# Kernel tuning notes

Measured on AMD Instinct MI355X. Metric: run time of the kernel, lower is better.

The kernel has to match this reference:

```python
import jax, jax.numpy as jnp
import numpy as np

D = 256; NH = 8; DH = D // NH; NL = 4; NP = 4; DFFN = 1024
SPATIAL = [(128, 128), (64, 64), (32, 32), (16, 16)]
LEN_IN = sum(h * w for h, w in SPATIAL)
N, LQ = 8, 1000


def _ln(x, g, b, eps=1e-5):
    m = jnp.mean(x, -1, keepdims=True)
    v = jnp.mean((x - m) ** 2, -1, keepdims=True)
    return (x - m) * jax.lax.rsqrt(v + eps) * g + b


def _ms_deform_core(value, loc, attn_w):
    # value (N,Len_in,NH,DH); loc (N,Lq,NH,NL,NP,2) in [0,1]; attn_w (N,Lq,NH,NL,NP)
    n, lq = loc.shape[0], loc.shape[1]
    out = jnp.zeros((n, NH, lq, DH), value.dtype)
    start = 0
    for l, (Hl, Wl) in enumerate(SPATIAL):
        v = value[:, start:start + Hl * Wl].transpose(0, 2, 1, 3)  # (N,NH,HW,DH)
        start += Hl * Wl
        # grid_sample-style mapping, align_corners=False, zero padding
        x = loc[:, :, :, l, :, 0] * Wl - 0.5  # (N,Lq,NH,NP)
        y = loc[:, :, :, l, :, 1] * Hl - 0.5
        x0 = jnp.floor(x); y0 = jnp.floor(y)
        lx = x - x0; ly = y - y0
        x0i = x0.astype(jnp.int32); y0i = y0.astype(jnp.int32)
        acc = jnp.zeros((n, NH, lq, NP, DH), value.dtype)
        for dy, dx, w in ((0, 0, (1 - ly) * (1 - lx)), (0, 1, (1 - ly) * lx),
                          (1, 0, ly * (1 - lx)), (1, 1, ly * lx)):
            xi = x0i + dx; yi = y0i + dy
            valid = ((xi >= 0) & (xi < Wl) & (yi >= 0) & (yi < Hl)).astype(value.dtype)
            idx = jnp.clip(yi, 0, Hl - 1) * Wl + jnp.clip(xi, 0, Wl - 1)  # (N,Lq,NH,NP)
            idx = idx.transpose(0, 2, 1, 3).reshape(n, NH, lq * NP)
            g = jnp.take_along_axis(v, idx[..., None], axis=2).reshape(n, NH, lq, NP, DH)
            acc = acc + g * (w * valid).transpose(0, 2, 1, 3)[..., None]
        out = out + jnp.sum(acc * attn_w[:, :, :, l].transpose(0, 2, 1, 3)[..., None], axis=3)
    return out.transpose(0, 2, 1, 3).reshape(n, lq, D)


def setup_inputs() -> dict:
    key = jax.random.key(0)
    ks = jax.random.split(key, 16)
    s = 0.02
    inp = {
        'tgt': jax.random.normal(ks[0], (N, LQ, D), jnp.float32),
        'query_pos': jax.random.normal(ks[1], (N, LQ, D), jnp.float32),
        'reference_points': jax.random.uniform(ks[2], (N, LQ, NL, 2), jnp.float32),
        'src': jax.random.normal(ks[3], (N, LEN_IN, D), jnp.float32),
        'spatial_shapes': jnp.array(SPATIAL, jnp.int32),
        'level_start_index': jnp.array(np.cumsum([0] + [h * w for h, w in SPATIAL[:-1]]), jnp.int32),
        # self-attention
        'sa_in_w': jax.random.normal(ks[4], (3 * D, D), jnp.float32) * s,
        'sa_in_b': jnp.zeros((3 * D,), jnp.float32),
        'sa_out_w': jax.random.normal(ks[5], (D, D), jnp.float32) * s,
        'sa_out_b': jnp.zeros((D,), jnp.float32),
        'norm2_g': jnp.ones((D,), jnp.float32), 'norm2_b': jnp.zeros((D,), jnp.float32),
        # MSDeformAttn
        'off_w': jax.random.normal(ks[6], (NH * NL * NP * 2, D), jnp.float32) * s,
        'off_b': jax.random.normal(ks[7], (NH * NL * NP * 2,), jnp.float32) * s,
        'aw_w': jax.random.normal(ks[8], (NH * NL * NP, D), jnp.float32) * s,
        'aw_b': jnp.zeros((NH * NL * NP,), jnp.float32),
        'val_w': jax.random.normal(ks[9], (D, D), jnp.float32) * s,
        'val_b': jnp.zeros((D,), jnp.float32),
        'outp_w': jax.random.normal(ks[10], (D, D), jnp.float32) * s,
        'outp_b': jnp.zeros((D,), jnp.float32),
        'norm1_g': jnp.ones((D,), jnp.float32), 'norm1_b': jnp.zeros((D,), jnp.float32),
        # FFN
        'ffn_w1': jax.random.normal(ks[11], (DFFN, D), jnp.float32) * s,
        'ffn_b1': jnp.zeros((DFFN,), jnp.float32),
        'ffn_w2': jax.random.normal(ks[12], (D, DFFN), jnp.float32) * s,
        'ffn_b2': jnp.zeros((D,), jnp.float32),
        'norm3_g': jnp.ones((D,), jnp.float32), 'norm3_b': jnp.zeros((D,), jnp.float32),
    }
    return inp


def reference(tgt, query_pos, reference_points, src, spatial_shapes, level_start_index,
              sa_in_w, sa_in_b, sa_out_w, sa_out_b, norm2_g, norm2_b,
              off_w, off_b, aw_w, aw_b, val_w, val_b, outp_w, outp_b, norm1_g, norm1_b,
              ffn_w1, ffn_b1, ffn_w2, ffn_b2, norm3_g, norm3_b):
    n, lq, _ = tgt.shape
    # ---- self-attention (q = k = tgt + pos, v = tgt), eval mode (dropout off)
    qk = tgt + query_pos
    wq, wk, wv = sa_in_w[:D], sa_in_w[D:2 * D], sa_in_w[2 * D:]
    bq, bk, bv = sa_in_b[:D], sa_in_b[D:2 * D], sa_in_b[2 * D:]
    q = (qk @ wq.T + bq).reshape(n, lq, NH, DH)
    k = (qk @ wk.T + bk).reshape(n, lq, NH, DH)
    v = (tgt @ wv.T + bv).reshape(n, lq, NH, DH)
    scores = jnp.einsum('bqhd,bkhd->bhqk', q, k) / np.sqrt(DH).astype(np.float32)
    attn = jax.nn.softmax(scores, axis=-1)
    sa = jnp.einsum('bhqk,bkhd->bqhd', attn, v).reshape(n, lq, D) @ sa_out_w.T + sa_out_b
    tgt = _ln(tgt + sa, norm2_g, norm2_b)
    # ---- multi-scale deformable cross-attention
    query = tgt + query_pos
    value = (src @ val_w.T + val_b).reshape(n, LEN_IN, NH, DH)
    offsets = (query @ off_w.T + off_b).reshape(n, lq, NH, NL, NP, 2)
    aw = (query @ aw_w.T + aw_b).reshape(n, lq, NH, NL * NP)
    aw = jax.nn.softmax(aw, axis=-1).reshape(n, lq, NH, NL, NP)
    # offset normalizer: (W_l, H_l)
    norm = jnp.stack([spatial_shapes[:, 1], spatial_shapes[:, 0]], -1).astype(tgt.dtype)
    loc = reference_points[:, :, None, :, None, :] + offsets / norm[None, None, None, :, None, :]
    ca = _ms_deform_core(value, loc, aw) @ outp_w.T + outp_b
    tgt = _ln(tgt + ca, norm1_g, norm1_b)
    # ---- FFN
    ff = jax.nn.relu(tgt @ ffn_w1.T + ffn_b1) @ ffn_w2.T + ffn_b2
    tgt = _ln(tgt + ff, norm3_g, norm3_b)
    return tgt
```

## Files before the change

### kernel.cpp

```cpp
#include <hip/hip_runtime.h>
#include <hip/hip_bf16.h>

#define D 256
#define NH 8
#define DH 32
#define NL 4
#define NP 4
#define DFFN 1024
#define LEN_IN 21760
#define NB 8
#define LQ 1000

typedef __hip_bfloat16 bf16;
typedef __attribute__((ext_vector_type(8))) short s8v;
typedef __attribute__((ext_vector_type(4))) float f4v;

template <typename T> __device__ inline T fromF(float x);
template <> __device__ inline float fromF<float>(float x) { return x; }
template <> __device__ inline bf16 fromF<bf16>(float x) { return __float2bfloat16(x); }

__device__ inline short bfr(float f) {
    unsigned u = __float_as_uint(f);
    u += 0x7fff + ((u >> 16) & 1);
    return (short)(u >> 16);
}
__device__ inline s8v pack8(float4 x, float4 y) {
    s8v r;
    r[0] = bfr(x.x); r[1] = bfr(x.y); r[2] = bfr(x.z); r[3] = bfr(x.w);
    r[4] = bfr(y.x); r[5] = bfr(y.y); r[6] = bfr(y.z); r[7] = bfr(y.w);
    return r;
}

__device__ inline unsigned cvtpk(float a, float b) {
    unsigned r;
    asm("v_cvt_pk_bf16_f32 %0, %1, %2" : "=v"(r) : "v"(a), "v"(b));
    return r;
}
__device__ inline s8v pkcvt8(float4 a, float4 b) {
    union { s8v v; unsigned u[4]; } r;
    r.u[0] = cvtpk(a.x, a.y);
    r.u[1] = cvtpk(a.z, a.w);
    r.u[2] = cvtpk(b.x, b.y);
    r.u[3] = cvtpk(b.z, b.w);
    return r.v;
}

__global__ __launch_bounds__(256) void pack_weights(const float* __restrict__ s0, const float* __restrict__ s1,
                                                    const float* __restrict__ s2, const float* __restrict__ s3,
                                                    const float* __restrict__ s4, const float* __restrict__ s5,
                                                    const float* __restrict__ s6, const float* __restrict__ s7,
                                                    bf16* __restrict__ dst) {
    int g = blockIdx.x * 256 + threadIdx.x;
    const float* s; int base;
    if      (g <  49152) { s = s0; base = 0;      }
    else if (g <  65536) { s = s1; base = 49152;  }
    else if (g <  81920) { s = s2; base = 65536;  }
    else if (g <  90112) { s = s3; base = 81920;  }
    else if (g < 106496) { s = s4; base = 90112;  }
    else if (g < 122880) { s = s5; base = 106496; }
    else if (g < 188416) { s = s6; base = 122880; }
    else                 { s = s7; base = 188416; }
    float4 v = ((const float4*)s)[g - base];
    short4 o; o.x = bfr(v.x); o.y = bfr(v.y); o.z = bfr(v.z); o.w = bfr(v.w);
    ((short4*)dst)[g] = o;
}

template <typename TA, typename TC, int MT, bool ADD2>
__global__ __launch_bounds__(256) void gemm_direct(const TA* __restrict__ A, const float* __restrict__ A2,
                                                   const bf16* __restrict__ W, const float* __restrict__ bias,
                                                   TC* __restrict__ C, int M, int N, int K, int do_relu) {
    const int tid = threadIdx.x;
    const int lane = tid & 63, wave = tid >> 6;
    const int fr = lane & 15, fq = lane >> 4;
    const int n0 = blockIdx.x * 128;
    const int wrow = blockIdx.y * (MT * 32) + (wave >> 1) * (MT * 16);
    const int wn = n0 + (wave & 1) * 64;
    (void)M;

    const TA* ap[MT];
    const float* a2p[MT];
#pragma unroll
    for (int i = 0; i < MT; ++i) {
        size_t r = (size_t)(wrow + i * 16 + fr);
        ap[i] = A + r * K + fq * 8;
        if constexpr (ADD2) a2p[i] = A2 + r * K + fq * 8;
    }
    const bf16* wp[4];
#pragma unroll
    for (int j = 0; j < 4; ++j) wp[j] = W + (size_t)(wn + j * 16 + fr) * K + fq * 8;

    f4v acc[MT][4];
#pragma unroll
    for (int i = 0; i < MT; ++i)
#pragma unroll
        for (int j = 0; j < 4; ++j) acc[i][j] = (f4v){0.f, 0.f, 0.f, 0.f};

    for (int k0 = 0; k0 < K; k0 += 32) {
        s8v bfv[4];
#pragma unroll
        for (int j = 0; j < 4; ++j) { bfv[j] = *(const s8v*)wp[j]; wp[j] += 32; }
        s8v af[MT];
#pragma unroll
        for (int i = 0; i < MT; ++i) {
            if constexpr (sizeof(TA) == 2) {
                af[i] = *(const s8v*)ap[i];
            } else {
                float4 x0 = *(const float4*)ap[i];
                float4 x1 = *(const float4*)(ap[i] + 4);
                if constexpr (ADD2) {
                    float4 y0 = *(const float4*)a2p[i];
                    float4 y1 = *(const float4*)(a2p[i] + 4);
                    x0.x += y0.x; x0.y += y0.y; x0.z += y0.z; x0.w += y0.w;
                    x1.x += y1.x; x1.y += y1.y; x1.z += y1.z; x1.w += y1.w;
                    a2p[i] += 32;
                }
                af[i] = pkcvt8(x0, x1);
            }
            ap[i] += 32;
        }
#pragma unroll
        for (int i = 0; i < MT; ++i)
#pragma unroll
            for (int j = 0; j < 4; ++j)
                acc[i][j] = __builtin_amdgcn_mfma_f32_16x16x32_bf16(af[i], bfv[j], acc[i][j], 0, 0, 0);
    }

#pragma unroll
    for (int j = 0; j < 4; ++j) {
        const int col = wn + j * 16 + fr;
        const float bb = bias[col];
#pragma unroll
        for (int i = 0; i < MT; ++i) {
            const int rbase = wrow + i * 16 + fq * 4;
#pragma unroll
            for (int r = 0; r < 4; ++r) {
                float v = acc[i][j][r] + bb;
                if (do_relu) v = fmaxf(v, 0.f);
                C[(size_t)(rbase + r) * N + col] = fromF<TC>(v);
            }
        }
    }
}

__global__ __launch_bounds__(256) void attn_mfma(const float* __restrict__ q, const float* __restrict__ k,
                                                 const float* __restrict__ v, float* __restrict__ out) {
    const int h = blockIdx.y, n = blockIdx.z;
    const int tid = threadIdx.x, wave = tid >> 6, lane = tid & 63;
    const int fr = lane & 15, fq = lane >> 4;
    __shared__ short Ks[32 * 40];
    __shared__ short Vt[32 * 40];
    __shared__ short Pl[4][16 * 40];
    const int q0 = blockIdx.x * 64 + wave * 16;

    s8v qfrag;
    {
        int qr = q0 + fr; if (qr >= LQ) qr = LQ - 1;
        const float* qp = q + ((size_t)(n * LQ + qr)) * D + h * DH + fq * 8;
        float4 t0 = *(const float4*)qp;
        float4 t1 = *(const float4*)(qp + 4);
        const float sc = 0.17677669529663687f;
        t0.x *= sc; t0.y *= sc; t0.z *= sc; t0.w *= sc;
        t1.x *= sc; t1.y *= sc; t1.z *= sc; t1.w *= sc;
        qfrag = pack8(t0, t1);
    }

    f4v O0 = {0.f, 0.f, 0.f, 0.f}, O1 = {0.f, 0.f, 0.f, 0.f};
    float mrow[4] = {-1e30f, -1e30f, -1e30f, -1e30f};
    float lrow[4] = {0.f, 0.f, 0.f, 0.f};

    for (int kt = 0; kt < LQ; kt += 32) {
        __syncthreads();
        {
            int key = tid >> 3, d4 = (tid & 7) * 4;
            int gk = kt + key; if (gk >= LQ) gk = LQ - 1;
            const float* kp = k + ((size_t)(n * LQ + gk)) * D + h * DH + d4;
            float4 t = *(const float4*)kp;
            short4 pk; pk.x = bfr(t.x); pk.y = bfr(t.y); pk.z = bfr(t.z); pk.w = bfr(t.w);
            *(short4*)&Ks[key * 40 + d4] = pk;
        }
        {
            int d = tid & 31, key0 = (tid >> 5) * 4;
            float vv[4];
#pragma unroll
            for (int i = 0; i < 4; ++i) {
                int gk = kt + key0 + i; if (gk >= LQ) gk = LQ - 1;
                vv[i] = v[((size_t)(n * LQ + gk)) * D + h * DH + d];
            }
            short4 pk; pk.x = bfr(vv[0]); pk.y = bfr(vv[1]); pk.z = bfr(vv[2]); pk.w = bfr(vv[3]);
            *(short4*)&Vt[d * 40 + key0] = pk;
        }
        __syncthreads();

        f4v s0 = {0.f, 0.f, 0.f, 0.f}, s1 = {0.f, 0.f, 0.f, 0.f};
        s8v kf0 = *(s8v*)&Ks[fr * 40 + fq * 8];
        s8v kf1 = *(s8v*)&Ks[(16 + fr) * 40 + fq * 8];
        s0 = __builtin_amdgcn_mfma_f32_16x16x32_bf16(qfrag, kf0, s0, 0, 0, 0);
        s1 = __builtin_amdgcn_mfma_f32_16x16x32_bf16(qfrag, kf1, s1, 0, 0, 0);
        const bool val0 = (kt + fr) < LQ, val1 = (kt + 16 + fr) < LQ;

        float p0[4], p1[4], alpha[4];
#pragma unroll
        for (int r = 0; r < 4; ++r) {
            float a = val0 ? s0[r] : -1e30f;
            float b = val1 ? s1[r] : -1e30f;
            float mx = fmaxf(a, b);
            mx = fmaxf(mx, __shfl_xor(mx, 1, 64));
            mx = fmaxf(mx, __shfl_xor(mx, 2, 64));
            mx = fmaxf(mx, __shfl_xor(mx, 4, 64));
            mx = fmaxf(mx, __shfl_xor(mx, 8, 64));
            float mnew = fmaxf(mrow[r], mx);
            float al = __expf(mrow[r] - mnew);
            float e0 = __expf(a - mnew);
            float e1 = __expf(b - mnew);
            float ps = e0 + e1;
            ps += __shfl_xor(ps, 1, 64);
            ps += __shfl_xor(ps, 2, 64);
            ps += __shfl_xor(ps, 4, 64);
            ps += __shfl_xor(ps, 8, 64);
            lrow[r] = lrow[r] * al + ps;
            mrow[r] = mnew;
            alpha[r] = al;
            p0[r] = e0; p1[r] = e1;
        }

        short* pw = Pl[wave];
#pragma unroll
        for (int r = 0; r < 4; ++r) {
            pw[(fq * 4 + r) * 40 + fr] = bfr(p0[r]);
            pw[(fq * 4 + r) * 40 + 16 + fr] = bfr(p1[r]);
        }
        __builtin_amdgcn_s_waitcnt(0);
        s8v pfrag = *(s8v*)&pw[fr * 40 + fq * 8];
        s8v vf0 = *(s8v*)&Vt[fr * 40 + fq * 8];
        s8v vf1 = *(s8v*)&Vt[(16 + fr) * 40 + fq * 8];
#pragma unroll
        for (int r = 0; r < 4; ++r) { O0[r] *= alpha[r]; O1[r] *= alpha[r]; }
        O0 = __builtin_amdgcn_mfma_f32_16x16x32_bf16(pfrag, vf0, O0, 0, 0, 0);
        O1 = __builtin_amdgcn_mfma_f32_16x16x32_bf16(pfrag, vf1, O1, 0, 0, 0);
    }

#pragma unroll
    for (int r = 0; r < 4; ++r) {
        int qrow = q0 + fq * 4 + r;
        if (qrow < LQ) {
            float inv = 1.0f / lrow[r];
            float* op = out + ((size_t)(n * LQ + qrow)) * D + h * DH;
            op[fr] = O0[r] * inv;
            op[16 + fr] = O1[r] * inv;
        }
    }
}

__global__ __launch_bounds__(256) void ln_res_kernel(const float* __restrict__ base, const float* __restrict__ delta,
                                                     const float* __restrict__ g, const float* __restrict__ b,
                                                     float* __restrict__ out) {
    __shared__ float scratch[8];
    const size_t row = blockIdx.x;
    const int d = threadIdx.x;
    float x = base[row * D + d] + delta[row * D + d];
    float s1 = x, s2 = x * x;
    for (int o = 32; o > 0; o >>= 1) {
        s1 += __shfl_down(s1, o, 64);
        s2 += __shfl_down(s2, o, 64);
    }
    const int w = threadIdx.x >> 6, lane = threadIdx.x & 63;
    if (lane == 0) { scratch[w] = s1; scratch[4 + w] = s2; }
    __syncthreads();
    s1 = scratch[0] + scratch[1] + scratch[2] + scratch[3];
    s2 = scratch[4] + scratch[5] + scratch[6] + scratch[7];
    float mean = s1 * (1.0f / 256.0f);
    float var = s2 * (1.0f / 256.0f) - mean * mean;
    float rstd = rsqrtf(var + 1e-5f);
    float y = (x - mean) * rstd * g[d] + b[d];
    out[row * D + d] = y;
}

__global__ __launch_bounds__(256) void aw_softmax_kernel(float* __restrict__ aw, int ngrp) {
    int t = blockIdx.x * 256 + threadIdx.x;
    if (t >= ngrp) return;
    float* p = aw + (size_t)t * 16;
    float m = p[0];
#pragma unroll
    for (int i = 1; i < 16; ++i) m = fmaxf(m, p[i]);
    float s = 0.f;
    float e[16];
#pragma unroll
    for (int i = 0; i < 16; ++i) { e[i] = __expf(p[i] - m); s += e[i]; }
    float inv = 1.0f / s;
#pragma unroll
    for (int i = 0; i < 16; ++i) p[i] = e[i] * inv;
}

__global__ __launch_bounds__(256) void deform_kernel(const bf16* __restrict__ value, const float* __restrict__ offs,
                                                     const float* __restrict__ aw, const float* __restrict__ refp,
                                                     float* __restrict__ out) {
    const int h = blockIdx.y, n = blockIdx.z;
    const int tid = threadIdx.x;
    const int wave = tid >> 6, lane = tid & 63;
    const int qi = blockIdx.x * 4 + wave;
    const int c = lane & 15;
    const int l = lane >> 4;
    const size_t row = (size_t)n * LQ + qi;
    const int W = 128 >> l, H = 128 >> l;
    const int START[4] = {0, 16384, 20480, 21504};
    const float invW = 1.0f / W, invH = 1.0f / H;

    const float rx = refp[(row * NL + l) * 2 + 0];
    const float ry = refp[(row * NL + l) * 2 + 1];
    const bf16* vbase = value + ((size_t)n * LEN_IN + START[l]) * D + h * DH + 2 * c;
    const float* offp = offs + row * D + (h * NL + l) * NP * 2;
    const float* awp = aw + row * 128 + h * 16 + l * 4;

    float acc0 = 0.f, acc1 = 0.f;
#pragma unroll
    for (int p = 0; p < 4; ++p) {
        float ox = offp[p * 2 + 0];
        float oy = offp[p * 2 + 1];
        float wa = awp[p];
        float x = (rx + ox * invW) * W - 0.5f;
        float y = (ry + oy * invH) * H - 0.5f;
        float xf = floorf(x), yf = floorf(y);
        float lx = x - xf, ly = y - yf;
        int x0 = (int)xf, y0 = (int)yf;
        int x1 = x0 + 1, y1 = y0 + 1;
        float vx0 = (x0 >= 0 && x0 < W) ? 1.f : 0.f;
        float vx1 = (x1 >= 0 && x1 < W) ? 1.f : 0.f;
        float vy0 = (y0 >= 0 && y0 < H) ? 1.f : 0.f;
        float vy1 = (y1 >= 0 && y1 < H) ? 1.f : 0.f;
        int x0c = min(max(x0, 0), W - 1), x1c = min(max(x1, 0), W - 1);
        int y0c = min(max(y0, 0), H - 1), y1c = min(max(y1, 0), H - 1);
        float w00 = wa * (1.f - ly) * (1.f - lx) * vy0 * vx0;
        float w01 = wa * (1.f - ly) * lx * vy0 * vx1;
        float w10 = wa * ly * (1.f - lx) * vy1 * vx0;
        float w11 = wa * ly * lx * vy1 * vx1;
        unsigned u00 = *(const unsigned*)(vbase + (size_t)(y0c * W + x0c) * D);
        unsigned u01 = *(const unsigned*)(vbase + (size_t)(y0c * W + x1c) * D);
        unsigned u10 = *(const unsigned*)(vbase + (size_t)(y1c * W + x0c) * D);
        unsigned u11 = *(const unsigned*)(vbase + (size_t)(y1c * W + x1c) * D);
        acc0 += w00 * __uint_as_float(u00 << 16) + w01 * __uint_as_float(u01 << 16)
              + w10 * __uint_as_float(u10 << 16) + w11 * __uint_as_float(u11 << 16);
        acc1 += w00 * __uint_as_float(u00 & 0xffff0000u) + w01 * __uint_as_float(u01 & 0xffff0000u)
              + w10 * __uint_as_float(u10 & 0xffff0000u) + w11 * __uint_as_float(u11 & 0xffff0000u);
    }
    acc0 += __shfl_xor(acc0, 16, 64); acc0 += __shfl_xor(acc0, 32, 64);
    acc1 += __shfl_xor(acc1, 16, 64); acc1 += __shfl_xor(acc1, 32, 64);
    if (l == 0) {
        float2 st = {acc0, acc1};
        *(float2*)(out + row * D + h * DH + 2 * c) = st;
    }
}

extern "C" void kernel_launch(void* const* d_in, const int* in_sizes, int n_in,
                              void* d_out, int out_size, void* d_ws, size_t ws_size,
                              hipStream_t stream) {
    const float* tgt = (const float*)d_in[0];
    const float* qpos = (const float*)d_in[1];
    const float* refp = (const float*)d_in[2];
    const float* src = (const float*)d_in[3];
    const float* sa_in_w = (const float*)d_in[6];
    const float* sa_in_b = (const float*)d_in[7];
    const float* sa_out_w = (const float*)d_in[8];
    const float* sa_out_b = (const float*)d_in[9];
    const float* norm2_g = (const float*)d_in[10];
    const float* norm2_b = (const float*)d_in[11];
    const float* off_w = (const float*)d_in[12];
    const float* off_b = (const float*)d_in[13];
    const float* aw_w = (const float*)d_in[14];
    const float* aw_b = (const float*)d_in[15];
    const float* val_w = (const float*)d_in[16];
    const float* val_b = (const float*)d_in[17];
    const float* outp_w = (const float*)d_in[18];
    const float* outp_b = (const float*)d_in[19];
    const float* norm1_g = (const float*)d_in[20];
    const float* norm1_b = (const float*)d_in[21];
    const float* ffn_w1 = (const float*)d_in[22];
    const float* ffn_b1 = (const float*)d_in[23];
    const float* ffn_w2 = (const float*)d_in[24];
    const float* ffn_b2 = (const float*)d_in[25];
    const float* norm3_g = (const float*)d_in[26];
    const float* norm3_b = (const float*)d_in[27];
    float* outp = (float*)d_out;

    const size_t NTOK = (size_t)NB * LQ;
    const size_t NE = NTOK * D;
    float* w = (float*)d_ws;
    size_t off = 0;
    auto alloc = [&](size_t n) { float* p = w + off; off += n; return p; };
    float* bufA = alloc(NE);
    float* bufB = alloc(NE);
    float* bufC = alloc(NE);
    float* bufD = alloc(NE);
    float* tgt2 = alloc(NE);
    float* tgt3 = alloc(NE);
    float* awb = alloc(NTOK * 128);
    bf16* mid = (bf16*)alloc(NTOK * DFFN / 2);
    bf16* value = (bf16*)alloc((size_t)NB * LEN_IN * D / 2);
    bf16* wb = (bf16*)alloc(507904);

    const bf16* wq    = wb;
    const bf16* wk    = wb + 65536;
    const bf16* wv    = wb + 131072;
    const bf16* wo    = wb + 196608;
    const bf16* woff  = wb + 262144;
    const bf16* waw   = wb + 327680;
    const bf16* wval  = wb + 360448;
    const bf16* woutp = wb + 425984;
    const bf16* wf1   = wb + 491520;
    const bf16* wf2   = wb + 753664;

    const int M8K = (int)NTOK;
    dim3 g8(2, M8K / 64);
    dim3 g8aw(1, M8K / 64);
    dim3 g8f1(DFFN / 128, M8K / 64);
    dim3 gVal(2, (NB * LEN_IN) / 128);

    pack_weights<<<992, 256, 0, stream>>>(sa_in_w, sa_out_w, off_w, aw_w, val_w, outp_w, ffn_w1, ffn_w2, wb);

    gemm_direct<float, float, 2, true><<<g8, 256, 0, stream>>>(tgt, qpos, wq, sa_in_b, bufB, M8K, D, D, 0);
    gemm_direct<float, float, 2, true><<<g8, 256, 0, stream>>>(tgt, qpos, wk, sa_in_b + 256, bufC, M8K, D, D, 0);
    gemm_direct<float, float, 2, false><<<g8, 256, 0, stream>>>(tgt, nullptr, wv, sa_in_b + 512, bufD, M8K, D, D, 0);
    attn_mfma<<<dim3((LQ + 63) / 64, NH, NB), 256, 0, stream>>>(bufB, bufC, bufD, bufA);
    gemm_direct<float, float, 2, false><<<g8, 256, 0, stream>>>(bufA, nullptr, wo, sa_out_b, bufB, M8K, D, D, 0);
    ln_res_kernel<<<NTOK, 256, 0, stream>>>(tgt, bufB, norm2_g, norm2_b, tgt2);

    gemm_direct<float, bf16, 4, false><<<gVal, 256, 0, stream>>>(src, nullptr, wval, val_b, value,
                                                                 NB * LEN_IN, D, D, 0);
    gemm_direct<float, float, 2, true><<<g8, 256, 0, stream>>>(tgt2, qpos, woff, off_b, bufD, M8K, D, D, 0);
    gemm_direct<float, float, 2, true><<<g8aw, 256, 0, stream>>>(tgt2, qpos, waw, aw_b, awb, M8K, 128, D, 0);
    aw_softmax_kernel<<<(int)(NTOK * NH + 255) / 256, 256, 0, stream>>>(awb, (int)(NTOK * NH));
    deform_kernel<<<dim3(LQ / 4, NH, NB), 256, 0, stream>>>(value, bufD, awb, refp, bufA);
    gemm_direct<float, float, 2, false><<<g8, 256, 0, stream>>>(bufA, nullptr, woutp, outp_b, bufB, M8K, D, D, 0);
    ln_res_kernel<<<NTOK, 256, 0, stream>>>(tgt2, bufB, norm1_g, norm1_b, tgt3);

    gemm_direct<float, bf16, 2, false><<<g8f1, 256, 0, stream>>>(tgt3, nullptr, wf1, ffn_b1, mid, M8K, DFFN, D, 1);
    gemm_direct<bf16, float, 2, false><<<g8, 256, 0, stream>>>(mid, nullptr, wf2, ffn_b2, bufC, M8K, D, DFFN, 0);
    ln_res_kernel<<<NTOK, 256, 0, stream>>>(tgt3, bufC, norm3_g, norm3_b, outp);
}
```

Before: 699.2 us.

## Stage value-projection A tiles through LDS via direct global-to-LDS loads; compile-time K

Adds a dedicated value-projection GEMM that copies 128x32 fp32 A tiles into swizzled shared memory with global_load_lds, then builds MFMA fragments from LDS instead of doing strided per-lane global loads. The generic GEMM also takes K as a template parameter, so its loops unroll fully for K=256 and partly for K=1024. The intent is better coalescing and higher memory throughput on the largest GEMM (174k rows), plus less loop overhead elsewhere. In exchange, the new kernel adds two barriers per K step with no double-buffering, and full unrolling may raise register pressure.

```diff
diff --git a/kernel.cpp b/kernel.cpp
--- a/kernel.cpp
+++ b/kernel.cpp
@@ -43,6 +43,13 @@
     r.u[2] = cvtpk(b.x, b.y);
     r.u[3] = cvtpk(b.z, b.w);
     return r.v;
+}
+
+__device__ __forceinline__ void gload_lds16(const void* gsrc, void* ldst) {
+    __builtin_amdgcn_global_load_lds(
+        (const __attribute__((address_space(1))) unsigned int*)gsrc,
+        (__attribute__((address_space(3))) unsigned int*)ldst,
+        16, 0, 0);
 }
 
 __global__ __launch_bounds__(256) void pack_weights(const float* __restrict__ s0, const float* __restrict__ s1,
@@ -65,29 +72,28 @@
     ((short4*)dst)[g] = o;
 }
 
-template <typename TA, typename TC, int MT, bool ADD2>
+template <typename TA, typename TC, int MT, bool ADD2, int KK>
 __global__ __launch_bounds__(256) void gemm_direct(const TA* __restrict__ A, const float* __restrict__ A2,
                                                    const bf16* __restrict__ W, const float* __restrict__ bias,
-                                                   TC* __restrict__ C, int M, int N, int K, int do_relu) {
+                                                   TC* __restrict__ C, int N, int do_relu) {
     const int tid = threadIdx.x;
     const int lane = tid & 63, wave = tid >> 6;
     const int fr = lane & 15, fq = lane >> 4;
     const int n0 = blockIdx.x * 128;
     const int wrow = blockIdx.y * (MT * 32) + (wave >> 1) * (MT * 16);
     const int wn = n0 + (wave & 1) * 64;
-    (void)M;
 
     const TA* ap[MT];
     const float* a2p[MT];
 #pragma unroll
     for (int i = 0; i < MT; ++i) {
         size_t r = (size_t)(wrow + i * 16 + fr);
-        ap[i] = A + r * K + fq * 8;
-        if constexpr (ADD2) a2p[i] = A2 + r * K + fq * 8;
+        ap[i] = A + r * KK + fq * 8;
+        if constexpr (ADD2) a2p[i] = A2 + r * KK + fq * 8;
     }
     const bf16* wp[4];
 #pragma unroll
-    for (int j = 0; j < 4; ++j) wp[j] = W + (size_t)(wn + j * 16 + fr) * K + fq * 8;
+    for (int j = 0; j < 4; ++j) wp[j] = W + (size_t)(wn + j * 16 + fr) * KK + fq * 8;
 
     f4v acc[MT][4];
 #pragma unroll
@@ -95,34 +101,40 @@
 #pragma unroll
         for (int j = 0; j < 4; ++j) acc[i][j] = (f4v){0.f, 0.f, 0.f, 0.f};
 
-    for (int k0 = 0; k0 < K; k0 += 32) {
+    auto step = [&](int k0) {
         s8v bfv[4];
 #pragma unroll
-        for (int j = 0; j < 4; ++j) { bfv[j] = *(const s8v*)wp[j]; wp[j] += 32; }
+        for (int j = 0; j < 4; ++j) bfv[j] = *(const s8v*)(wp[j] + k0);
         s8v af[MT];
 #pragma unroll
         for (int i = 0; i < MT; ++i) {
             if constexpr (sizeof(TA) == 2) {
-                af[i] = *(const s8v*)ap[i];
+                af[i] = *(const s8v*)((const bf16*)ap[i] + k0);
             } else {
-                float4 x0 = *(const float4*)ap[i];
-                float4 x1 = *(const float4*)(ap[i] + 4);
+                float4 x0 = *(const float4*)((const float*)ap[i] + k0);
+                float4 x1 = *(const float4*)((const float*)ap[i] + k0 + 4);
                 if constexpr (ADD2) {
-                    float4 y0 = *(const float4*)a2p[i];
-                    float4 y1 = *(const float4*)(a2p[i] + 4);
+                    float4 y0 = *(const float4*)(a2p[i] + k0);
+                    float4 y1 = *(const float4*)(a2p[i] + k0 + 4);
                     x0.x += y0.x; x0.y += y0.y; x0.z += y0.z; x0.w += y0.w;
                     x1.x += y1.x; x1.y += y1.y; x1.z += y1.z; x1.w += y1.w;
-                    a2p[i] += 32;
                 }
                 af[i] = pkcvt8(x0, x1);
             }
-            ap[i] += 32;
         }
 #pragma unroll
         for (int i = 0; i < MT; ++i)
 #pragma unroll
             for (int j = 0; j < 4; ++j)
                 acc[i][j] = __builtin_amdgcn_mfma_f32_16x16x32_bf16(af[i], bfv[j], acc[i][j], 0, 0, 0);
+    };
+
+    if constexpr (KK <= 256) {
+#pragma unroll
+        for (int k0 = 0; k0 < KK; k0 += 32) step(k0);
+    } else {
+#pragma unroll 4
+        for (int k0 = 0; k0 < KK; k0 += 32) step(k0);
     }
 
 #pragma unroll
@@ -137,6 +149,84 @@
                 float v = acc[i][j][r] + bb;
                 if (do_relu) v = fmaxf(v, 0.f);
                 C[(size_t)(rbase + r) * N + col] = fromF<TC>(v);
+            }
+        }
+    }
+}
+
+__global__ __launch_bounds__(256) void gemm_val(const float* __restrict__ A, const bf16* __restrict__ W,
+                                                const float* __restrict__ bias, bf16* __restrict__ C) {
+    __shared__ float As[4096];
+    const int tid = threadIdx.x;
+    const int lane = tid & 63, wave = tid >> 6;
+    const int fr = lane & 15, fq = lane >> 4;
+    const int m0 = blockIdx.y * 128;
+    const int wm = (wave >> 1) * 64;
+    const int wn = blockIdx.x * 128 + (wave & 1) * 64;
+
+    int srow[4], soff[4];
+#pragma unroll
+    for (int g = 0; g < 4; ++g) {
+        int s = g * 4096 + tid * 16;
+        int r = s >> 7;
+        srow[g] = r;
+        soff[g] = (s & 127) ^ ((r & 7) << 4);
+    }
+    int rb[4][2];
+#pragma unroll
+    for (int i = 0; i < 4; ++i) {
+        int r2 = wm + i * 16 + fr;
+        rb[i][0] = r2 * 128 + ((fq * 32) ^ ((r2 & 7) << 4));
+        rb[i][1] = r2 * 128 + ((fq * 32 + 16) ^ ((r2 & 7) << 4));
+    }
+    const bf16* wp[4];
+#pragma unroll
+    for (int j = 0; j < 4; ++j) wp[j] = W + (size_t)(wn + j * 16 + fr) * 256 + fq * 8;
+
+    f4v acc[4][4];
+#pragma unroll
+    for (int i = 0; i < 4; ++i)
+#pragma unroll
+        for (int j = 0; j < 4; ++j) acc[i][j] = (f4v){0.f, 0.f, 0.f, 0.f};
+
+#pragma unroll
+    for (int kk = 0; kk < 8; ++kk) {
+        const int k0 = kk * 32;
+        __syncthreads();
+#pragma unroll
+        for (int g = 0; g < 4; ++g) {
+            const char* gsrc = (const char*)(A + (size_t)(m0 + srow[g]) * 256 + k0) + soff[g];
+            gload_lds16(gsrc, (char*)As + g * 4096 + tid * 16);
+        }
+        __syncthreads();
+        s8v bfv[4];
+#pragma unroll
+        for (int j = 0; j < 4; ++j) bfv[j] = *(const s8v*)(wp[j] + k0);
+        s8v af[4];
+#pragma unroll
+        for (int i = 0; i < 4; ++i) {
+            float4 x0 = *(const float4*)((const char*)As + rb[i][0]);
+            float4 x1 = *(const float4*)((const char*)As + rb[i][1]);
+            af[i] = pkcvt8(x0, x1);
+        }
+#pragma unroll
+        for (int i = 0; i < 4; ++i)
+#pragma unroll
+            for (int j = 0; j < 4; ++j)
+                acc[i][j] = __builtin_amdgcn_mfma_f32_16x16x32_bf16(af[i], bfv[j], acc[i][j], 0, 0, 0);
+    }
+
+#pragma unroll
+    for (int j = 0; j < 4; ++j) {
+        const int col = wn + j * 16 + fr;
+        const float bb = bias[col];
+#pragma unroll
+        for (int i = 0; i < 4; ++i) {
+            const int rbase = m0 + wm + i * 16 + fq * 4;
+#pragma unroll
+            for (int r = 0; r < 4; ++r) {
+                float v = acc[i][j][r] + bb;
+                C[(size_t)(rbase + r) * 256 + col] = fromF<bf16>(v);
             }
         }
     }
@@ -416,23 +506,22 @@
 
     pack_weights<<<992, 256, 0, stream>>>(sa_in_w, sa_out_w, off_w, aw_w, val_w, outp_w, ffn_w1, ffn_w2, wb);
 
-    gemm_direct<float, float, 2, true><<<g8, 256, 0, stream>>>(tgt, qpos, wq, sa_in_b, bufB, M8K, D, D, 0);
-    gemm_direct<float, float, 2, true><<<g8, 256, 0, stream>>>(tgt, qpos, wk, sa_in_b + 256, bufC, M8K, D, D, 0);
-    gemm_direct<float, float, 2, false><<<g8, 256, 0, stream>>>(tgt, nullptr, wv, sa_in_b + 512, bufD, M8K, D, D, 0);
+    gemm_direct<float, float, 2, true, 256><<<g8, 256, 0, stream>>>(tgt, qpos, wq, sa_in_b, bufB, D, 0);
+    gemm_direct<float, float, 2, true, 256><<<g8, 256, 0, stream>>>(tgt, qpos, wk, sa_in_b + 256, bufC, D, 0);
+    gemm_direct<float, float, 2, false, 256><<<g8, 256, 0, stream>>>(tgt, nullptr, wv, sa_in_b + 512, bufD, D, 0);
     attn_mfma<<<dim3((LQ + 63) / 64, NH, NB), 256, 0, stream>>>(bufB, bufC, bufD, bufA);
-    gemm_direct<float, float, 2, false><<<g8, 256, 0, stream>>>(bufA, nullptr, wo, sa_out_b, bufB, M8K, D, D, 0);
+    gemm_direct<float, float, 2, false, 256><<<g8, 256, 0, stream>>>(bufA, nullptr, wo, sa_out_b, bufB, D, 0);
     ln_res_kernel<<<NTOK, 256, 0, stream>>>(tgt, bufB, norm2_g, norm2_b, tgt2);
 
-    gemm_direct<float, bf16, 4, false><<<gVal, 256, 0, stream>>>(src, nullptr, wval, val_b, value,
-                                                                 NB * LEN_IN, D, D, 0);
-    gemm_direct<float, float, 2, true><<<g8, 256, 0, stream>>>(tgt2, qpos, woff, off_b, bufD, M8K, D, D, 0);
-    gemm_direct<float, float, 2, true><<<g8aw, 256, 0, stream>>>(tgt2, qpos, waw, aw_b, awb, M8K, 128, D, 0);
+    gemm_val<<<gVal, 256, 0, stream>>>(src, wval, val_b, value);
+    gemm_direct<float, float, 2, true, 256><<<g8, 256, 0, stream>>>(tgt2, qpos, woff, off_b, bufD, D, 0);
+    gemm_direct<float, float, 2, true, 256><<<g8aw, 256, 0, stream>>>(tgt2, qpos, waw, aw_b, awb, 128, 0);
     aw_softmax_kernel<<<(int)(NTOK * NH + 255) / 256, 256, 0, stream>>>(awb, (int)(NTOK * NH));
     deform_kernel<<<dim3(LQ / 4, NH, NB), 256, 0, stream>>>(value, bufD, awb, refp, bufA);
-    gemm_direct<float, float, 2, false><<<g8, 256, 0, stream>>>(bufA, nullptr, woutp, outp_b, bufB, M8K, D, D, 0);
+    gemm_direct<float, float, 2, false, 256><<<g8, 256, 0, stream>>>(bufA, nullptr, woutp, outp_b, bufB, D, 0);
     ln_res_kernel<<<NTOK, 256, 0, stream>>>(tgt2, bufB, norm1_g, norm1_b, tgt3);
 
-    gemm_direct<float, bf16, 2, false><<<g8f1, 256, 0, stream>>>(tgt3, nullptr, wf1, ffn_b1, mid, M8K, DFFN, D, 1);
-    gemm_direct<bf16, float, 2, false><<<g8, 256, 0, stream>>>(mid, nullptr, wf2, ffn_b2, bufC, M8K, D, DFFN, 0);
+    gemm_direct<float, bf16, 2, false, 256><<<g8f1, 256, 0, stream>>>(tgt3, nullptr, wf1, ffn_b1, mid, DFFN, 1);
+    gemm_direct<bf16, float, 2, false, 1024><<<g8, 256, 0, stream>>>(mid, nullptr, wf2, ffn_b2, bufC, D, 0);
     ln_res_kernel<<<NTOK, 256, 0, stream>>>(tgt3, bufC, norm3_g, norm3_b, outp);
 }
```

Result: faster. 652.1 us (-6.7%).
